# Performance work log

Measured on AMD Instinct MI355X. Metric: run time of the kernel, lower is better.

## Reference

```python
import jax, jax.numpy as jnp
import numpy as np

CH = 512
GROUPS = 32
EPS = 1e-6


def setup_inputs() -> dict:
    key = jax.random.key(0)
    ks = jax.random.split(key, 12)
    b, c, h, w = 4, CH, 64, 64
    std = 1.0 / np.sqrt(c)
    return {
        "x": jax.random.normal(ks[0], (b, c, h, w), dtype=jnp.float32),
        "norm_gamma": jnp.ones((c,), jnp.float32),
        "norm_beta": jnp.zeros((c,), jnp.float32),
        "wq": jax.random.normal(ks[1], (c, c), jnp.float32) * std,
        "bq": jax.random.normal(ks[2], (c,), jnp.float32) * 0.01,
        "wk": jax.random.normal(ks[3], (c, c), jnp.float32) * std,
        "bk": jax.random.normal(ks[4], (c,), jnp.float32) * 0.01,
        "wv": jax.random.normal(ks[5], (c, c), jnp.float32) * std,
        "bv": jax.random.normal(ks[6], (c,), jnp.float32) * 0.01,
        "wo": jax.random.normal(ks[7], (c, c), jnp.float32) * std,
        "bo": jax.random.normal(ks[8], (c,), jnp.float32) * 0.01,
    }


def _group_norm(x, gamma, beta):
    b, c, h, w = x.shape
    xg = x.reshape(b, GROUPS, c // GROUPS, h, w)
    mean = xg.mean(axis=(2, 3, 4), keepdims=True)
    var = xg.var(axis=(2, 3, 4), keepdims=True)
    xn = ((xg - mean) * jax.lax.rsqrt(var + EPS)).reshape(b, c, h, w)
    return xn * gamma[None, :, None, None] + beta[None, :, None, None]


def reference(x, norm_gamma, norm_beta, wq, bq, wk, bk, wv, bv, wo, bo):
    b, c, h, w = x.shape
    hn = _group_norm(x, norm_gamma, norm_beta)
    hs = hn.reshape(b, c, h * w)  # [b, c, n]
    # 1x1 convs == per-pixel matmuls over channel dim (weight[out,in])
    q = jnp.einsum('oc,bcn->bno', wq, hs) + bq  # [b, n, c]
    k = jnp.einsum('oc,bcn->bon', wk, hs) + bk[None, :, None]  # [b, c, n]
    v = jnp.einsum('oc,bcn->bno', wv, hs) + bv  # [b, n, c]
    scale = c ** (-0.5)
    attn = jax.nn.softmax(jnp.einsum('bnc,bcm->bnm', q, k) * scale, axis=-1)
    out = jnp.einsum('bnm,bmc->bnc', attn, v)  # [b, n, c]
    out = jnp.einsum('oc,bnc->bon', wo, out) + bo[None, :, None]  # [b, c, n]
    return x + out.reshape(b, c, h, w)
```

## Files before the change

### kernel.cpp

```cpp
#include <hip/hip_runtime.h>
#include <hip/hip_bf16.h>
#include <cstdint>

typedef __bf16 bf16;
typedef __bf16 bf16x8 __attribute__((ext_vector_type(8)));
typedef __bf16 bf16x4 __attribute__((ext_vector_type(4)));
typedef float f32x4 __attribute__((ext_vector_type(4)));

__device__ __forceinline__ void gld_lds16(const void* g, void* l) {
  __builtin_amdgcn_global_load_lds((const __attribute__((address_space(1))) void*)g,
                                   (__attribute__((address_space(3))) void*)l, 16, 0, 0);
}

enum { BIAS_NONE = 0, BIAS_COL = 1, BIAS_ROW = 2, BIAS_QK = 3 };
enum { OUT_BF16 = 0, OUT_F32_RESID = 1 };

template<int BIAS_MODE, int OUT_MODE>
__global__ __launch_bounds__(256)
void gemm_bt(const bf16* __restrict__ A, long sA, int lda,
             const bf16* __restrict__ Bm, long sB, int ldb,
             void* __restrict__ Cv, long sC, int ldc,
             const float* __restrict__ bias, const float* __restrict__ bias2,
             const float* __restrict__ resid, long sR,
             int K, float scale)
{
  const int bm = blockIdx.x, bn = blockIdx.y, bz = blockIdx.z;
  const char* Ab = (const char*)(A + (long)bz * sA);
  const char* Bb = (const char*)(Bm + (long)bz * sB);
  const int tid = threadIdx.x;
  const int wave = tid >> 6, lane = tid & 63;
  const int wr = wave >> 1, wc = wave & 1;

  __shared__ __attribute__((aligned(128))) char lds[32768];
  char* ldsA = lds;
  char* ldsB = lds + 16384;

  uint32_t aoff[4], boff[4];
#pragma unroll
  for (int i = 0; i < 4; ++i) {
    uint32_t ra = (uint32_t)(wr * 64 + i * 16 + (lane & 15));
    uint32_t la = ra * 128u + (uint32_t)((lane >> 4) << 4);
    aoff[i] = la ^ ((la >> 3) & 0x70u);
    uint32_t rb = (uint32_t)(wc * 64 + i * 16 + (lane & 15));
    uint32_t lb = rb * 128u + (uint32_t)((lane >> 4) << 4);
    boff[i] = lb ^ ((lb >> 3) & 0x70u);
  }
  uint32_t srow[4], sinb[4];
#pragma unroll
  for (int t = 0; t < 4; ++t) {
    uint32_t paddr = (uint32_t)(((wave * 4 + t) * 64 + lane) * 16);
    uint32_t laddr = paddr ^ ((paddr >> 3) & 0x70u);
    srow[t] = laddr >> 7;
    sinb[t] = laddr & 127u;
  }

  const long ldab = (long)lda * 2, ldbb = (long)ldb * 2;
  const long arow0 = (long)bm * 128, brow0 = (long)bn * 128;
  f32x4 acc[4][4] = {};
  const int nK = K >> 6;
  for (int kt = 0; kt < nK; ++kt) {
    const long k0b = (long)kt * 128;
#pragma unroll
    for (int t = 0; t < 4; ++t) {
      gld_lds16(Ab + (arow0 + srow[t]) * ldab + k0b + sinb[t], ldsA + (wave * 4 + t) * 1024);
      gld_lds16(Bb + (brow0 + srow[t]) * ldbb + k0b + sinb[t], ldsB + (wave * 4 + t) * 1024);
    }
    __syncthreads();
#pragma unroll
    for (int kk = 0; kk < 2; ++kk) {
      bf16x8 af[4], bfr[4];
#pragma unroll
      for (int i = 0; i < 4; ++i) {
        af[i]  = *(const bf16x8*)(ldsA + (aoff[i] ^ (kk << 6)));
        bfr[i] = *(const bf16x8*)(ldsB + (boff[i] ^ (kk << 6)));
      }
#pragma unroll
      for (int mi = 0; mi < 4; ++mi)
#pragma unroll
        for (int ni = 0; ni < 4; ++ni)
          acc[mi][ni] = __builtin_amdgcn_mfma_f32_16x16x32_bf16(af[mi], bfr[ni], acc[mi][ni], 0, 0, 0);
    }
    __syncthreads();
  }

  const int cl = lane & 15, rq = lane >> 4;
  const long row0 = (long)bm * 128 + wr * 64;
  const long col0 = (long)bn * 128 + wc * 64;

  if constexpr (OUT_MODE == OUT_F32_RESID) {
    float* Co = (float*)Cv + (long)bz * sC;
    const float* X = resid + (long)bz * sR;
#pragma unroll
    for (int mi = 0; mi < 4; ++mi)
#pragma unroll
      for (int ni = 0; ni < 4; ++ni) {
        const long col = col0 + ni * 16 + cl;
#pragma unroll
        for (int j = 0; j < 4; ++j) {
          const long row = row0 + mi * 16 + rq * 4 + j;
          Co[row * ldc + col] = acc[mi][ni][j] + bias[row] + X[row * ldc + col];
        }
      }
  } else if constexpr (BIAS_MODE == BIAS_QK) {
    const bool isq = (col0 < 512);
    bf16* base = (bf16*)Cv + (long)bz * sC + (isq ? 0 : sR);
    const long csub = isq ? 0 : 512;
#pragma unroll
    for (int mi = 0; mi < 4; ++mi)
#pragma unroll
      for (int ni = 0; ni < 4; ++ni) {
        const long col = col0 + ni * 16 + cl;
        const float bc = isq ? bias[col] * scale : bias2[col - 512];
        const float vs = isq ? scale : 1.f;
#pragma unroll
        for (int j = 0; j < 4; ++j) {
          const long row = row0 + mi * 16 + rq * 4 + j;
          base[row * ldc + (col - csub)] = (bf16)(acc[mi][ni][j] * vs + bc);
        }
      }
  } else {
    bf16* Co = (bf16*)Cv + (long)bz * sC;
#pragma unroll
    for (int mi = 0; mi < 4; ++mi)
#pragma unroll
      for (int ni = 0; ni < 4; ++ni) {
        const long col = col0 + ni * 16 + cl;
        float bc = 0.f;
        if (BIAS_MODE == BIAS_COL) bc = bias[col] * scale;
#pragma unroll
        for (int j = 0; j < 4; ++j) {
          const long row = row0 + mi * 16 + rq * 4 + j;
          float v = acc[mi][ni][j] * (BIAS_MODE == BIAS_COL ? scale : 1.f) + bc;
          if (BIAS_MODE == BIAS_ROW) v += bias[row];
          Co[row * ldc + col] = (bf16)v;
        }
      }
  }
}

__global__ __launch_bounds__(256, 2)
void gemm_pv6(const bf16* __restrict__ S, long sA,
              const bf16* __restrict__ Vm, long sB,
              bf16* __restrict__ O, long sC, int swz)
{
  constexpr int T = 64;
  extern __shared__ char lds[];
  char* ldsA = lds;
  char* ldsB = lds + 16384;

  int bm, bn, bz;
  if (swz) {
    const int bid = blockIdx.x;
    const int xcd = bid & 7;
    bz = xcd >> 1;
    bn = (bid >> 3) & 1;
    bm = ((bid >> 4) << 1) | (xcd & 1);
  } else { bm = blockIdx.x; bn = blockIdx.y; bz = blockIdx.z; }

  const char* Ab = (const char*)(S + (long)bz * sA) + (long)bm * 64 * 8192;
  const char* Bb = (const char*)(Vm + (long)bz * sB) + (long)bn * 256 * 8192;
  const int tid = threadIdx.x, wave = tid >> 6, lane = tid & 63;
  const int lg = lane >> 4, l15 = lane & 15;

  const uint32_t ar0 = (uint32_t)(tid >> 3), ac16 = (uint32_t)((tid & 7) * 16);
  const uint32_t aswz = (ar0 & 7) << 4;

  const uint32_t bdst0 = (uint32_t)tid * 16;

  uint32_t aO[4], bO[4];
#pragma unroll
  for (int mi = 0; mi < 4; ++mi) {
    uint32_t r = (uint32_t)(mi * 16 + l15);
    aO[mi] = r * 128 + (((uint32_t)(lg * 16)) ^ ((r & 7) << 4));
  }
#pragma unroll
  for (int ni = 0; ni < 4; ++ni) {
    uint32_t r = (uint32_t)(wave * 64 + ni * 16 + l15);
    bO[ni] = r * 128 + (((uint32_t)(lg * 16)) ^ ((r & 7) << 4));
  }

  f32x4 acc[4][4] = {};
  float lsum0 = 0.f, lsum1 = 0.f;

  auto stageB = [&](uint32_t nb, int t) {
#pragma unroll
    for (int j = 0; j < 8; ++j) {
      uint32_t row = (uint32_t)(j * 32) + ar0;
      gld_lds16(Bb + (long)row * 8192 + (long)t * 128 + (ac16 ^ ((row & 7) << 4)),
                ldsB + nb * 32768 + (uint32_t)(j * 4096) + bdst0);
    }
  };
  auto loadA0 = [&](int t) -> bf16x8 {
    return *(const bf16x8*)(Ab + (long)ar0 * 8192 + (long)t * 128 + ac16);
  };
  auto loadA1 = [&](int t) -> bf16x8 {
    return *(const bf16x8*)(Ab + (long)(32 + ar0) * 8192 + (long)t * 128 + ac16);
  };
  auto writeA = [&](uint32_t nb, bf16x8 s0, bf16x8 s1) {
    bf16x8 p0, p1;
#pragma unroll
    for (int j = 0; j < 8; ++j) {
      float e0 = __expf((float)s0[j]);
      float e1 = __expf((float)s1[j]);
      p0[j] = (bf16)e0; p1[j] = (bf16)e1;
      lsum0 += e0; lsum1 += e1;
    }
    *(bf16x8*)(ldsA + nb * 8192 + ar0 * 128 + (ac16 ^ aswz)) = p0;
    *(bf16x8*)(ldsA + nb * 8192 + (32 + ar0) * 128 + (ac16 ^ aswz)) = p1;
  };

  {
    bf16x8 s0 = loadA0(0), s1 = loadA1(0);
    stageB(0, 0);
    writeA(0, s0, s1);
  }
  bf16x8 an0 = loadA0(1), an1 = loadA1(1);
  stageB(1, 1);
  asm volatile("s_waitcnt vmcnt(10)" ::: "memory");
  asm volatile("s_waitcnt lgkmcnt(0)" ::: "memory");
  __builtin_amdgcn_sched_barrier(0);
  __builtin_amdgcn_s_barrier();

  for (int t = 0; t < T; ++t) {
    const uint32_t cur = (uint32_t)(t & 1), nxt = cur ^ 1u;

    bf16x8 af[4][2], bfr[4][2];
#pragma unroll
    for (int mi = 0; mi < 4; ++mi)
#pragma unroll
      for (int kk = 0; kk < 2; ++kk)
        af[mi][kk] = *(const bf16x8*)(ldsA + ((cur * 8192 + aO[mi]) ^ (uint32_t)(kk << 6)));
#pragma unroll
    for (int ni = 0; ni < 4; ++ni)
#pragma unroll
      for (int kk = 0; kk < 2; ++kk)
        bfr[ni][kk] = *(const bf16x8*)(ldsB + ((cur * 32768 + bO[ni]) ^ (uint32_t)(kk << 6)));

    if (t + 1 < T) writeA(nxt, an0, an1);

    asm volatile("s_waitcnt lgkmcnt(0)" ::: "memory");
    __builtin_amdgcn_sched_barrier(0);
    __builtin_amdgcn_s_barrier();

    if (t + 2 < T) {
      an0 = loadA0(t + 2);
      an1 = loadA1(t + 2);
      stageB(cur, t + 2);
    }

    __builtin_amdgcn_s_setprio(1);
#pragma unroll
    for (int mi = 0; mi < 4; ++mi)
#pragma unroll
      for (int ni = 0; ni < 4; ++ni)
#pragma unroll
        for (int kk = 0; kk < 2; ++kk)
          acc[mi][ni] = __builtin_amdgcn_mfma_f32_16x16x32_bf16(af[mi][kk], bfr[ni][kk], acc[mi][ni], 0, 0, 0);
    __builtin_amdgcn_s_setprio(0);

    if (t + 1 < T) {
      if (t + 2 < T) asm volatile("s_waitcnt vmcnt(10)" ::: "memory");
      else           asm volatile("s_waitcnt vmcnt(0)" ::: "memory");
      __builtin_amdgcn_s_barrier();
    }
  }

  lsum0 += __shfl_xor(lsum0, 1, 64);
  lsum0 += __shfl_xor(lsum0, 2, 64);
  lsum0 += __shfl_xor(lsum0, 4, 64);
  lsum1 += __shfl_xor(lsum1, 1, 64);
  lsum1 += __shfl_xor(lsum1, 2, 64);
  lsum1 += __shfl_xor(lsum1, 4, 64);
  float* Lrow = (float*)ldsA;
  if ((tid & 7) == 0) {
    Lrow[ar0] = lsum0;
    Lrow[32 + ar0] = lsum1;
  }
  __syncthreads();

  bf16* Co = O + (long)bz * sC + (long)bm * 64 * 512 + (long)bn * 256;
#pragma unroll
  for (int mi = 0; mi < 4; ++mi)
#pragma unroll
    for (int j = 0; j < 4; ++j) {
      const int row = mi * 16 + lg * 4 + j;
      const float invL = 1.f / Lrow[row];
#pragma unroll
      for (int ni = 0; ni < 4; ++ni) {
        const int col = wave * 64 + ni * 16 + l15;
        Co[(long)row * 512 + col] = (bf16)(acc[mi][ni][j] * invL);
      }
    }
}

__global__ __launch_bounds__(256)
void gn_stats(const float* __restrict__ x, float* __restrict__ stats)
{
  const int bg = blockIdx.x;
  const float4* px = (const float4*)(x + (long)bg * 65536);
  float s1 = 0.f, s2 = 0.f;
  for (int i = threadIdx.x; i < 16384; i += 256) {
    float4 f = px[i];
    s1 += f.x + f.y + f.z + f.w;
    s2 += f.x * f.x + f.y * f.y + f.z * f.z + f.w * f.w;
  }
#pragma unroll
  for (int d = 32; d > 0; d >>= 1) {
    s1 += __shfl_xor(s1, d, 64);
    s2 += __shfl_xor(s2, d, 64);
  }
  __shared__ float r1[4], r2[4];
  const int wave = threadIdx.x >> 6, lane = threadIdx.x & 63;
  if (lane == 0) { r1[wave] = s1; r2[wave] = s2; }
  __syncthreads();
  if (threadIdx.x == 0) {
    float t1 = r1[0] + r1[1] + r1[2] + r1[3];
    float t2 = r2[0] + r2[1] + r2[2] + r2[3];
    float mean = t1 * (1.f / 65536.f);
    float var  = t2 * (1.f / 65536.f) - mean * mean;
    stats[bg * 2]     = mean;
    stats[bg * 2 + 1] = rsqrtf(var + 1e-6f);
  }
}

__global__ __launch_bounds__(256)
void gn_apply(const float* __restrict__ x, const float* __restrict__ stats,
              const float* __restrict__ gamma, const float* __restrict__ beta,
              bf16* __restrict__ hn)
{
  const int b = blockIdx.y;
  const int n0 = blockIdx.x * 64;
  __shared__ __attribute__((aligned(16))) char lt[65536];
  const int tid = threadIdx.x;
  for (int i = 0; i < 32; ++i) {
    int f = i * 256 + tid;
    int c = f >> 4;
    int n4 = f & 15;
    float4 xv = *(const float4*)(x + (((long)b * 512 + c) * 4096) + n0 + n4 * 4);
    int g = c >> 4;
    float mean = stats[(b * 32 + g) * 2];
    float rstd = stats[(b * 32 + g) * 2 + 1];
    float ga = gamma[c], be = beta[c];
    float y[4];
    y[0] = (xv.x - mean) * rstd * ga + be;
    y[1] = (xv.y - mean) * rstd * ga + be;
    y[2] = (xv.z - mean) * rstd * ga + be;
    y[3] = (xv.w - mean) * rstd * ga + be;
    uint32_t cb = (uint32_t)(c * 2);
#pragma unroll
    for (int jj = 0; jj < 4; ++jj) {
      uint32_t nl = (uint32_t)(n4 * 4 + jj);
      uint32_t phys = nl * 1024u + (cb ^ (((nl >> 2) & 7u) << 4));
      *(bf16*)(lt + phys) = (bf16)y[jj];
    }
  }
  __syncthreads();
  for (int i = 0; i < 16; ++i) {
    int j = i * 256 + tid;
    uint32_t row = (uint32_t)(j >> 6);
    uint32_t m = (uint32_t)(j & 63);
    uint32_t phys = row * 1024u + ((m * 16u) ^ (((row >> 2) & 7u) << 4));
    uint4 val = *(const uint4*)(lt + phys);
    *(uint4*)((char*)(hn + ((long)b * 4096 + n0 + row) * 512) + m * 16) = val;
  }
}

__global__ __launch_bounds__(256)
void conv_w4(const float* __restrict__ w0, const float* __restrict__ w1,
             const float* __restrict__ w2, const float* __restrict__ w3,
             bf16* __restrict__ dst)
{
  const int z = blockIdx.y;
  const float* src = (z == 0) ? w0 : (z == 1) ? w1 : (z == 2) ? w2 : w3;
  const int i = blockIdx.x * 256 + threadIdx.x;
  float4 f = ((const float4*)src)[i];
  bf16x4 o;
  o[0] = (bf16)f.x; o[1] = (bf16)f.y; o[2] = (bf16)f.z; o[3] = (bf16)f.w;
  ((bf16x4*)(dst))[(long)z * 65536 + i] = o;
}

extern "C" void kernel_launch(void* const* d_in, const int* in_sizes, int n_in,
                              void* d_out, int out_size, void* d_ws, size_t ws_size,
                              hipStream_t stream)
{
  const float* x     = (const float*)d_in[0];
  const float* gamma = (const float*)d_in[1];
  const float* beta  = (const float*)d_in[2];
  const float* wq = (const float*)d_in[3];
  const float* bq = (const float*)d_in[4];
  const float* wk = (const float*)d_in[5];
  const float* bk = (const float*)d_in[6];
  const float* wv = (const float*)d_in[7];
  const float* bv = (const float*)d_in[8];
  const float* wo = (const float*)d_in[9];
  const float* bo = (const float*)d_in[10];
  float* out = (float*)d_out;

  char* ws = (char*)d_ws;
  bf16* hn  = (bf16*)(ws + 0);
  bf16* q   = (bf16*)(ws + 16777216);
  bf16* k   = (bf16*)(ws + 33554432);
  bf16* v   = (bf16*)(ws + 50331648);
  bf16* O   = (bf16*)(ws + 67108864);
  bf16* wqb = (bf16*)(ws + 83886080);
  bf16* wvb = (bf16*)(ws + 84934656);
  bf16* wob = (bf16*)(ws + 85458944);
  float* gstats = (float*)(ws + 85983232);
  bf16* S   = (bf16*)(ws + 85984256);

  const long sBC = 2097152;
  const long sS1 = 16777216;
  const long K_OFS = 8388608;
  const float scale = 0.044194173824159216f;

  const int LDS_PV = 81920;
  hipFuncSetAttribute(reinterpret_cast<const void*>(gemm_pv6),
                      hipFuncAttributeMaxDynamicSharedMemorySize, LDS_PV);

  conv_w4<<<dim3(256, 4), 256, 0, stream>>>(wq, wk, wv, wo, wqb);
  gn_stats<<<128, 256, 0, stream>>>(x, gstats);
  gn_apply<<<dim3(64, 4), 256, 0, stream>>>(x, gstats, gamma, beta, hn);

  gemm_bt<BIAS_QK, OUT_BF16><<<dim3(32, 8, 4), 256, 0, stream>>>(
      hn, sBC, 512, wqb, 0, 512, q, sBC, 512,
      bq, bk, nullptr, K_OFS, 512, scale);
  gemm_bt<BIAS_ROW, OUT_BF16><<<dim3(4, 32, 4), 256, 0, stream>>>(
      wvb, 0, 512, hn, sBC, 512, v, sBC, 4096,
      bv, nullptr, nullptr, 0, 512, 1.f);

  const bool tier1 = ws_size >= (size_t)220202112;
  if (tier1) {
    gemm_bt<BIAS_NONE, OUT_BF16><<<dim3(32, 32, 4), 256, 0, stream>>>(
        q, sBC, 512, k, sBC, 512, S, sS1, 4096,
        nullptr, nullptr, nullptr, 0, 512, 1.f);
    gemm_pv6<<<dim3(512, 1, 1), 256, LDS_PV, stream>>>(
        S, sS1, v, sBC, O, sBC, 1);
  } else {
    for (int b = 0; b < 4; ++b) {
      gemm_bt<BIAS_NONE, OUT_BF16><<<dim3(32, 32, 1), 256, 0, stream>>>(
          q + b * sBC, 0, 512, k + b * sBC, 0, 512, S, 0, 4096,
          nullptr, nullptr, nullptr, 0, 512, 1.f);
      gemm_pv6<<<dim3(64, 2, 1), 256, LDS_PV, stream>>>(
          S, 0, v + b * sBC, 0, O + b * sBC, 0, 0);
    }
  }

  gemm_bt<BIAS_ROW, OUT_F32_RESID><<<dim3(4, 32, 4), 256, 0, stream>>>(
      wob, 0, 512, O, sBC, 512, out, sBC, 4096,
      bo, nullptr, x, sBC, 512, 1.f);
}
```

Before: 274.5 us.

## Move exp into QK^T epilogue and restructure PV kernel pipeline to one barrier

The exponentiation of attention scores moves from the PV kernel's A-staging path into the epilogue of the QK^T GEMM, so the PV kernel only sums the precomputed probabilities. The PV main loop is reordered to issue the next tile's B stage and A write before the LDS fragment reads, which removes the mid-iteration barrier and leaves one barrier per iteration. The intent is to cut VALU work and a sync point from the PV inner loop. The risk is that the row sums now use bf16-rounded exp values, and that writing into the next buffer while other waves still read the current one depends on the barrier placement being correct.

```diff
diff --git a/kernel.cpp b/kernel.cpp
--- a/kernel.cpp
+++ b/kernel.cpp
@@ -13,7 +13,7 @@
 }
 
 enum { BIAS_NONE = 0, BIAS_COL = 1, BIAS_ROW = 2, BIAS_QK = 3 };
-enum { OUT_BF16 = 0, OUT_F32_RESID = 1 };
+enum { OUT_BF16 = 0, OUT_F32_RESID = 1, OUT_EXP = 2 };
 
 template<int BIAS_MODE, int OUT_MODE>
 __global__ __launch_bounds__(256)
@@ -132,6 +132,7 @@
           const long row = row0 + mi * 16 + rq * 4 + j;
           float v = acc[mi][ni][j] * (BIAS_MODE == BIAS_COL ? scale : 1.f) + bc;
           if (BIAS_MODE == BIAS_ROW) v += bias[row];
+          if constexpr (OUT_MODE == OUT_EXP) v = __expf(v);
           Co[row * ldc + col] = (bf16)v;
         }
       }
@@ -139,7 +140,7 @@
 }
 
 __global__ __launch_bounds__(256, 2)
-void gemm_pv6(const bf16* __restrict__ S, long sA,
+void gemm_pv7(const bf16* __restrict__ P, long sA,
               const bf16* __restrict__ Vm, long sB,
               bf16* __restrict__ O, long sC, int swz)
 {
@@ -157,7 +158,7 @@
     bm = ((bid >> 4) << 1) | (xcd & 1);
   } else { bm = blockIdx.x; bn = blockIdx.y; bz = blockIdx.z; }
 
-  const char* Ab = (const char*)(S + (long)bz * sA) + (long)bm * 64 * 8192;
+  const char* Ab = (const char*)(P + (long)bz * sA) + (long)bm * 64 * 8192;
   const char* Bb = (const char*)(Vm + (long)bz * sB) + (long)bn * 256 * 8192;
   const int tid = threadIdx.x, wave = tid >> 6, lane = tid & 63;
   const int lg = lane >> 4, l15 = lane & 15;
@@ -196,27 +197,21 @@
   auto loadA1 = [&](int t) -> bf16x8 {
     return *(const bf16x8*)(Ab + (long)(32 + ar0) * 8192 + (long)t * 128 + ac16);
   };
-  auto writeA = [&](uint32_t nb, bf16x8 s0, bf16x8 s1) {
-    bf16x8 p0, p1;
+  auto writeA = [&](uint32_t nb, bf16x8 p0, bf16x8 p1) {
 #pragma unroll
     for (int j = 0; j < 8; ++j) {
-      float e0 = __expf((float)s0[j]);
-      float e1 = __expf((float)s1[j]);
-      p0[j] = (bf16)e0; p1[j] = (bf16)e1;
-      lsum0 += e0; lsum1 += e1;
+      lsum0 += (float)p0[j];
+      lsum1 += (float)p1[j];
     }
     *(bf16x8*)(ldsA + nb * 8192 + ar0 * 128 + (ac16 ^ aswz)) = p0;
     *(bf16x8*)(ldsA + nb * 8192 + (32 + ar0) * 128 + (ac16 ^ aswz)) = p1;
   };
 
-  {
-    bf16x8 s0 = loadA0(0), s1 = loadA1(0);
-    stageB(0, 0);
-    writeA(0, s0, s1);
-  }
-  bf16x8 an0 = loadA0(1), an1 = loadA1(1);
-  stageB(1, 1);
-  asm volatile("s_waitcnt vmcnt(10)" ::: "memory");
+  bf16x8 an0 = loadA0(0), an1 = loadA1(0);
+  stageB(0, 0);
+  writeA(0, an0, an1);
+  an0 = loadA0(1); an1 = loadA1(1);
+  asm volatile("s_waitcnt vmcnt(2)" ::: "memory");
   asm volatile("s_waitcnt lgkmcnt(0)" ::: "memory");
   __builtin_amdgcn_sched_barrier(0);
   __builtin_amdgcn_s_barrier();
@@ -224,6 +219,10 @@
   for (int t = 0; t < T; ++t) {
     const uint32_t cur = (uint32_t)(t & 1), nxt = cur ^ 1u;
 
+    if (t + 1 < T) stageB(nxt, t + 1);
+    if (t + 1 < T) writeA(nxt, an0, an1);
+    if (t + 2 < T) { an0 = loadA0(t + 2); an1 = loadA1(t + 2); }
+
     bf16x8 af[4][2], bfr[4][2];
 #pragma unroll
     for (int mi = 0; mi < 4; ++mi)
@@ -235,18 +234,6 @@
 #pragma unroll
       for (int kk = 0; kk < 2; ++kk)
         bfr[ni][kk] = *(const bf16x8*)(ldsB + ((cur * 32768 + bO[ni]) ^ (uint32_t)(kk << 6)));
-
-    if (t + 1 < T) writeA(nxt, an0, an1);
-
-    asm volatile("s_waitcnt lgkmcnt(0)" ::: "memory");
-    __builtin_amdgcn_sched_barrier(0);
-    __builtin_amdgcn_s_barrier();
-
-    if (t + 2 < T) {
-      an0 = loadA0(t + 2);
-      an1 = loadA1(t + 2);
-      stageB(cur, t + 2);
-    }
 
     __builtin_amdgcn_s_setprio(1);
 #pragma unroll
@@ -259,8 +246,10 @@
     __builtin_amdgcn_s_setprio(0);
 
     if (t + 1 < T) {
-      if (t + 2 < T) asm volatile("s_waitcnt vmcnt(10)" ::: "memory");
+      if (t + 2 < T) asm volatile("s_waitcnt vmcnt(2)" ::: "memory");
       else           asm volatile("s_waitcnt vmcnt(0)" ::: "memory");
+      asm volatile("s_waitcnt lgkmcnt(0)" ::: "memory");
+      __builtin_amdgcn_sched_barrier(0);
       __builtin_amdgcn_s_barrier();
     }
   }
@@ -414,7 +403,7 @@
   const float scale = 0.044194173824159216f;
 
   const int LDS_PV = 81920;
-  hipFuncSetAttribute(reinterpret_cast<const void*>(gemm_pv6),
+  hipFuncSetAttribute(reinterpret_cast<const void*>(gemm_pv7),
                       hipFuncAttributeMaxDynamicSharedMemorySize, LDS_PV);
 
   conv_w4<<<dim3(256, 4), 256, 0, stream>>>(wq, wk, wv, wo, wqb);
@@ -430,17 +419,17 @@
 
   const bool tier1 = ws_size >= (size_t)220202112;
   if (tier1) {
-    gemm_bt<BIAS_NONE, OUT_BF16><<<dim3(32, 32, 4), 256, 0, stream>>>(
+    gemm_bt<BIAS_NONE, OUT_EXP><<<dim3(32, 32, 4), 256, 0, stream>>>(
         q, sBC, 512, k, sBC, 512, S, sS1, 4096,
         nullptr, nullptr, nullptr, 0, 512, 1.f);
-    gemm_pv6<<<dim3(512, 1, 1), 256, LDS_PV, stream>>>(
+    gemm_pv7<<<dim3(512, 1, 1), 256, LDS_PV, stream>>>(
         S, sS1, v, sBC, O, sBC, 1);
   } else {
     for (int b = 0; b < 4; ++b) {
-      gemm_bt<BIAS_NONE, OUT_BF16><<<dim3(32, 32, 1), 256, 0, stream>>>(
+      gemm_bt<BIAS_NONE, OUT_EXP><<<dim3(32, 32, 1), 256, 0, stream>>>(
           q + b * sBC, 0, 512, k + b * sBC, 0, 512, S, 0, 4096,
           nullptr, nullptr, nullptr, 0, 512, 1.f);
-      gemm_pv6<<<dim3(64, 2, 1), 256, LDS_PV, stream>>>(
+      gemm_pv7<<<dim3(64, 2, 1), 256, LDS_PV, stream>>>(
           S, 0, v + b * sBC, 0, O + b * sBC, 0, 0);
     }
   }
```

Result: no change. 269.2 us (median of 3 runs) (-1.9%).
